# Kernel tuning notes

Hardware: AMD Instinct MI355X
Metric: run time of the kernel (lower is better)

Reference implementation:

```python
import jax, jax.numpy as jnp
import numpy as np

DEPTH = 16          # levels in the complete binary tree
D_IN = 256
H = 256
K = 2               # n_children
N_NODES = 2 ** DEPTH - 1  # 65535, heap/level order: children of node p at level l are (2p, 2p+1) at level l+1


def setup_inputs() -> dict:
    key = jax.random.key(0)
    ks = jax.random.split(key, 14)
    s = 0.05
    emb = jax.random.normal(ks[0], (N_NODES, D_IN), dtype=jnp.float32)
    mk = lambda k, shape: (jax.random.normal(k, shape, dtype=jnp.float32) * s)
    return {
        "emb": emb,
        "W_i": mk(ks[1], (H, D_IN)), "b_i": mk(ks[2], (H,)), "U_i": mk(ks[3], (K, H, H)),
        "W_o": mk(ks[4], (H, D_IN)), "b_o": mk(ks[5], (H,)), "U_o": mk(ks[6], (K, H, H)),
        "W_u": mk(ks[7], (H, D_IN)), "b_u": mk(ks[8], (H,)), "U_u": mk(ks[9], (K, H, H)),
        "W_f": mk(ks[10], (H, D_IN)), "b_f": mk(ks[11], (H,)), "U_f": mk(ks[12], (K, H, H)),
    }


def _node_batch(x, ch_h, ch_c, W_i, b_i, U_i, W_o, b_o, U_o, W_u, b_u, U_u, W_f, b_f, U_f):
    # x: [n, D_IN]; ch_h, ch_c: [n, K, H]
    # Linear: x @ W.T + b (torch layout W=[out,in]); U_k h = h @ U[k].T
    def gate(W, b, U):
        return x @ W.T + b + jnp.einsum("nkh,kdh->nd", ch_h, U)
    i = jax.nn.sigmoid(gate(W_i, b_i, U_i))
    o = jax.nn.sigmoid(gate(W_o, b_o, U_o))
    u = jnp.tanh(gate(W_u, b_u, U_u))
    # per-child forget gates: f_k = sigmoid(W_f x + U_f[k] h_k)
    f = jax.nn.sigmoid((x @ W_f.T + b_f)[:, None, :] + jnp.einsum("nkh,kdh->nkd", ch_h, U_f))
    c = i * u + jnp.sum(f * ch_c, axis=1)
    h = o * jnp.tanh(c)
    return h, c


def reference(emb, W_i, b_i, U_i, W_o, b_o, U_o, W_u, b_u, U_u, W_f, b_f, U_f):
    params = (W_i, b_i, U_i, W_o, b_o, U_o, W_u, b_u, U_u, W_f, b_f, U_f)
    # leaves: level DEPTH-1, zero children (matches zero-padding in node_forward)
    n = 2 ** (DEPTH - 1)
    start = n - 1
    zeros = jnp.zeros((n, K, H), dtype=emb.dtype)
    h, c = _node_batch(emb[start:start + n], zeros, zeros, *params)
    # bottom-up over internal levels; children of position p are (2p, 2p+1) in level below
    for l in range(DEPTH - 2, -1, -1):
        n = 2 ** l
        start = n - 1
        ch_h = h.reshape(n, K, H)
        ch_c = c.reshape(n, K, H)
        h, c = _node_batch(emb[start:start + n], ch_h, ch_c, *params)
    return h[0], c[0]  # root (hidden, cell), each [H]
```

## Files before the change

### kernel.cpp

```cpp
#include <hip/hip_runtime.h>
#include <hip/hip_bf16.h>
#include <cstdint>
#include <cstddef>


typedef __attribute__((ext_vector_type(8))) __bf16 bf16x8;
typedef __attribute__((ext_vector_type(4))) float floatx4;

#define TB 64

__device__ __forceinline__ float sigf(float x) { return 1.0f / (1.0f + __expf(-x)); }

__device__ __forceinline__ void load_lds16(const void* g, void* l) {
    __builtin_amdgcn_global_load_lds(
        (const __attribute__((address_space(1))) unsigned int*)g,
        (__attribute__((address_space(3))) unsigned int*)l, 16, 0, 0);
}

__global__ void pack_weights(const float* __restrict__ Wi, const float* __restrict__ bi, const float* __restrict__ Ui,
                             const float* __restrict__ Wo, const float* __restrict__ bo, const float* __restrict__ Uo,
                             const float* __restrict__ Wu, const float* __restrict__ bu, const float* __restrict__ Uu,
                             const float* __restrict__ Wf, const float* __restrict__ bf, const float* __restrict__ Uf,
                             __hip_bfloat16* __restrict__ Wpack, float* __restrict__ biasv)
{
    int m = blockIdx.x;
    int d = blockIdx.y;
    int k = threadIdx.x;
    const float* tbl[12] = {Wi, Wo, Wu, Wf,
                            Ui, Uo, Uu, Uf,
                            Ui + 65536, Uo + 65536, Uu + 65536, Uf + 65536};
    Wpack[((size_t)m * 256 + d) * 256 + k] = __float2bfloat16(tbl[m][d * 256 + k]);
    if (m < 4 && k == 0) {
        const float* bt[4] = {bi, bo, bu, bf};
        biasv[m * 256 + d] = bt[m][d];
    }
}

__global__ void convert_f32_bf16(const float* __restrict__ in, __hip_bfloat16* __restrict__ out, int n4)
{
    int i = blockIdx.x * 256 + threadIdx.x;
    if (i >= n4) return;
    float4 v = ((const float4*)in)[i];
    __hip_bfloat16 tmp[4];
    tmp[0] = __float2bfloat16(v.x);
    tmp[1] = __float2bfloat16(v.y);
    tmp[2] = __float2bfloat16(v.z);
    tmp[3] = __float2bfloat16(v.w);
    *(ushort4*)(out + (size_t)i * 4) = *(const ushort4*)tmp;
}

__global__ __launch_bounds__(256) void gemm_zx(
    const __hip_bfloat16* __restrict__ embB,
    const __hip_bfloat16* __restrict__ Wpack,
    const float* __restrict__ biasv,
    float* __restrict__ preZ,
    int M)
{
    __shared__ __hip_bfloat16 sA[64 * 32];
    __shared__ __hip_bfloat16 sB[64 * 32];
    const int t = threadIdx.x;
    const int s = blockIdx.x >> 2;
    const int d0 = (blockIdx.x & 3) * 64;
    const int bm0 = blockIdx.y * 64;
    const int lane = t & 63, w = t >> 6, lrow = lane & 15, q = lane >> 4;

    floatx4 acc[4];
    #pragma unroll
    for (int mt = 0; mt < 4; ++mt) acc[mt] = (floatx4){0.f, 0.f, 0.f, 0.f};

    for (int kk = 0; kk < 8; ++kk) {
        const int k0 = kk * 32;
        {
            int r = t >> 2, kc = t & 3;
            load_lds16(embB + (size_t)(bm0 + r) * 256 + k0 + kc * 8, &sA[t * 8]);
            load_lds16(Wpack + (size_t)(s * 256 + d0 + r) * 256 + k0 + kc * 8, &sB[t * 8]);
        }
        __syncthreads();
        bf16x8 af[4];
        #pragma unroll
        for (int mt = 0; mt < 4; ++mt)
            af[mt] = *(const bf16x8*)&sA[(mt * 16 + lrow) * 32 + q * 8];
        bf16x8 bfr = *(const bf16x8*)&sB[(w * 16 + lrow) * 32 + q * 8];
        #pragma unroll
        for (int mt = 0; mt < 4; ++mt)
            acc[mt] = __builtin_amdgcn_mfma_f32_16x16x32_bf16(af[mt], bfr, acc[mt], 0, 0, 0);
        __syncthreads();
    }

    const int d = d0 + w * 16 + lrow;
    const float bv = biasv[s * 256 + d];
    #pragma unroll
    for (int mt = 0; mt < 4; ++mt)
        #pragma unroll
        for (int rr = 0; rr < 4; ++rr) {
            int m = bm0 + mt * 16 + q * 4 + rr;
            if (m < M) preZ[(size_t)m * 1024 + s * 256 + d] = acc[mt][rr] + bv;
        }
}

template<int NS, int NP>
__global__ __launch_bounds__(256) void fused_level3(
    const __hip_bfloat16* __restrict__ embX,
    const __hip_bfloat16* __restrict__ hprev,
    const float* __restrict__ cprev,
    const __hip_bfloat16* __restrict__ Wpack,
    const float* __restrict__ biasv,
    __hip_bfloat16* __restrict__ hout,
    float* __restrict__ cout,
    int M)
{
    __shared__ __hip_bfloat16 sA[64 * 64];
    __shared__ __hip_bfloat16 sB[NS * 64 * 64];
    const int t = threadIdx.x;
    const int dchunk = blockIdx.x;
    const int bm0 = blockIdx.y * 64;
    const int lane = t & 63;
    const int w = t >> 6;
    const int lrow = lane & 15;
    const int q = lane >> 4;

    floatx4 accS[3][4];
    floatx4 accF[NP][4];
    #pragma unroll
    for (int s = 0; s < 3; ++s)
        #pragma unroll
        for (int mt = 0; mt < 4; ++mt) accS[s][mt] = (floatx4){0.f, 0.f, 0.f, 0.f};
    #pragma unroll
    for (int p = 0; p < NP; ++p)
        #pragma unroll
        for (int mt = 0; mt < 4; ++mt) accF[p][mt] = (floatx4){0.f, 0.f, 0.f, 0.f};

    #pragma unroll
    for (int p = 0; p < NP; ++p) {
        const __hip_bfloat16* Abase = (p == 0) ? embX : hprev;
        const int astride = (p == 0) ? 256 : 512;
        const int aoff = (p == 0) ? 0 : (p - 1) * 256;
        for (int kk = 0; kk < 4; ++kk) {
            const int k0 = kk * 64;
            #pragma unroll
            for (int rep = 0; rep < 2; ++rep) {
                int C = rep * 256 + t;
                int r = C >> 3, c0 = C & 7;
                load_lds16(Abase + (size_t)(bm0 + r) * astride + aoff + k0 + (c0 ^ (r & 7)) * 8,
                           &sA[C * 8]);
            }
            #pragma unroll
            for (int rep = 0; rep < NS * 2; ++rep) {
                int C = rep * 256 + t;
                int s = C >> 9, r = (C >> 3) & 63, c0 = C & 7;
                load_lds16(Wpack + (size_t)((p * 4 + s) * 256 + dchunk * 64 + r) * 256
                                 + k0 + (c0 ^ (r & 7)) * 8,
                           &sB[C * 8]);
            }
            __syncthreads();

            bf16x8 af[2][4];
            #pragma unroll
            for (int ks = 0; ks < 2; ++ks)
                #pragma unroll
                for (int mt = 0; mt < 4; ++mt)
                    af[ks][mt] = *(const bf16x8*)&sA[(mt * 16 + lrow) * 64
                                                     + (((ks * 4 + q) ^ (lrow & 7)) * 8)];
            #pragma unroll
            for (int s = 0; s < NS; ++s) {
                #pragma unroll
                for (int ks = 0; ks < 2; ++ks) {
                    bf16x8 bfr = *(const bf16x8*)&sB[(s * 64 + w * 16 + lrow) * 64
                                                     + (((ks * 4 + q) ^ (lrow & 7)) * 8)];
                    if (s < 3) {
                        #pragma unroll
                        for (int mt = 0; mt < 4; ++mt)
                            accS[s][mt] = __builtin_amdgcn_mfma_f32_16x16x32_bf16(af[ks][mt], bfr, accS[s][mt], 0, 0, 0);
                    } else {
                        #pragma unroll
                        for (int mt = 0; mt < 4; ++mt)
                            accF[p][mt] = __builtin_amdgcn_mfma_f32_16x16x32_bf16(af[ks][mt], bfr, accF[p][mt], 0, 0, 0);
                    }
                }
            }
            __syncthreads();
        }
    }

    const int d = dchunk * 64 + w * 16 + lrow;
    const float bI = biasv[d];
    const float bO = biasv[256 + d];
    const float bU = biasv[512 + d];
    const float bF = (NS == 4) ? biasv[768 + d] : 0.0f;
    #pragma unroll
    for (int mt = 0; mt < 4; ++mt) {
        #pragma unroll
        for (int rr = 0; rr < 4; ++rr) {
            const int m = bm0 + mt * 16 + q * 4 + rr;
            if (m >= M) continue;
            float iv = sigf(accS[0][mt][rr] + bI);
            float ov = sigf(accS[1][mt][rr] + bO);
            float uv = tanhf(accS[2][mt][rr] + bU);
            float c;
            if (NS == 4) {
                float fx = accF[0][mt][rr];
                float fl = sigf(fx + accF[NP >= 2 ? 1 : 0][mt][rr] + bF);
                float fr = sigf(fx + accF[NP >= 3 ? 2 : 0][mt][rr] + bF);
                c = iv * uv + fl * cprev[(size_t)m * 512 + d]
                            + fr * cprev[(size_t)m * 512 + 256 + d];
            } else {
                c = iv * uv;
            }
            cout[(size_t)m * 256 + d] = c;
            hout[(size_t)m * 256 + d] = __float2bfloat16(ov * tanhf(c));
        }
    }
}

__global__ __launch_bounds__(256) void tail_levels(
    __hip_bfloat16* __restrict__ hbuf, float* __restrict__ cbuf,
    const __hip_bfloat16* __restrict__ Wpack,
    const float* __restrict__ preZ,
    unsigned* __restrict__ bar, float* __restrict__ out)
{
    __shared__ __hip_bfloat16 sB[8 * 16 * 256];
    const int bid = blockIdx.x;
    const int t = threadIdx.x;
    const int dt = bid & 15;
    const int g = bid >> 4;
    const int w = t >> 6, lane = t & 63, lrow = lane & 15, q = lane >> 4;

    for (int rnd = 0; rnd < 16; ++rnd) {
        int C = rnd * 256 + t;
        int q8k = C & 31, r = (C >> 5) & 15, m8 = C >> 9;
        load_lds16(Wpack + (size_t)((4 + m8) * 256 + dt * 16 + r) * 256 + (q8k ^ (r & 7)) * 8,
                   &sB[(size_t)C * 8]);
    }
    __syncthreads();

    const int d = dt * 16 + lrow;
    unsigned barnum = 0;
    unsigned snum = 0;

    for (int l = 10; l >= 0; --l) {
        if (l <= 7 && g != 0) break;

        const int n = 1 << l;
        const int start = n - 1;
        const int startc = 2 * n - 1;
        const __hip_bfloat16* hp = hbuf + (size_t)startc * 256;
        const float* cp = cbuf + (size_t)startc * 256;
        __hip_bfloat16* ho = hbuf + (size_t)start * 256;
        float* co = cbuf + (size_t)start * 256;
        const int nmt = (n + 15) >> 4;
        const int slot   = (l > 7) ? (g * 4 + w) : w;
        const int stride = (l > 7) ? 16 : 4;

        for (int mt = slot; mt < nmt; mt += stride) {
            const int m0 = mt * 16;
            bf16x8 af[2][8];
            #pragma unroll
            for (int p = 0; p < 2; ++p)
                #pragma unroll
                for (int kk = 0; kk < 8; ++kk)
                    af[p][kk] = *(const bf16x8*)(hp + (size_t)(m0 + lrow) * 512 + p * 256 + kk * 32 + q * 8);
            float zi[4][4], clr[2][4];
            #pragma unroll
            for (int rr = 0; rr < 4; ++rr) {
                int m = m0 + q * 4 + rr;
                #pragma unroll
                for (int s = 0; s < 4; ++s)
                    zi[s][rr] = preZ[(size_t)(start + m) * 1024 + s * 256 + d];
                clr[0][rr] = cp[(size_t)m * 512 + d];
                clr[1][rr] = cp[(size_t)m * 512 + 256 + d];
            }

            floatx4 accS[3], accF1, accF2;
            #pragma unroll
            for (int s = 0; s < 3; ++s)
                accS[s] = (floatx4){zi[s][0], zi[s][1], zi[s][2], zi[s][3]};
            accF1 = (floatx4){0.f, 0.f, 0.f, 0.f};
            accF2 = (floatx4){0.f, 0.f, 0.f, 0.f};

            #pragma unroll
            for (int p = 0; p < 2; ++p)
                #pragma unroll
                for (int kk = 0; kk < 8; ++kk)
                    #pragma unroll
                    for (int s = 0; s < 4; ++s) {
                        bf16x8 bfr = *(const bf16x8*)&sB[((p * 4 + s) * 16 + lrow) * 256
                                                         + (((kk * 4 + q) ^ (lrow & 7)) * 8)];
                        if (s < 3)
                            accS[s] = __builtin_amdgcn_mfma_f32_16x16x32_bf16(af[p][kk], bfr, accS[s], 0, 0, 0);
                        else if (p == 0)
                            accF1 = __builtin_amdgcn_mfma_f32_16x16x32_bf16(af[p][kk], bfr, accF1, 0, 0, 0);
                        else
                            accF2 = __builtin_amdgcn_mfma_f32_16x16x32_bf16(af[p][kk], bfr, accF2, 0, 0, 0);
                    }

            #pragma unroll
            for (int rr = 0; rr < 4; ++rr) {
                int m = m0 + q * 4 + rr;
                if (m >= n) continue;
                float iv = sigf(accS[0][rr]);
                float ov = sigf(accS[1][rr]);
                float uv = tanhf(accS[2][rr]);
                float fx = zi[3][rr];
                float fl = sigf(fx + accF1[rr]);
                float fr = sigf(fx + accF2[rr]);
                float c = iv * uv + fl * clr[0][rr] + fr * clr[1][rr];
                float hv = ov * tanhf(c);
                if (l == 0) {
                    out[d] = hv;
                    out[256 + d] = c;
                } else {
                    co[(size_t)m * 256 + d] = c;
                    ho[(size_t)m * 256 + d] = __float2bfloat16(hv);
                }
            }
        }

        if (l > 0) {
            __syncthreads();
            if (l > 7) {
                ++barnum;
                if (t == 0) {
                    unsigned v = __hip_atomic_fetch_add(&bar[0], 1, __ATOMIC_ACQ_REL,
                                                        __HIP_MEMORY_SCOPE_AGENT) + 1;
                    if (v == barnum * 64u) {
                        __hip_atomic_fetch_add(&bar[64], 1, __ATOMIC_RELEASE,
                                               __HIP_MEMORY_SCOPE_AGENT);
                    } else {
                        while (__hip_atomic_load(&bar[64], __ATOMIC_RELAXED,
                                                 __HIP_MEMORY_SCOPE_AGENT) < barnum)
                            __builtin_amdgcn_s_sleep(1);
                    }
                }
            } else {
                ++snum;
                if (t == 0) {
                    unsigned v = __hip_atomic_fetch_add(&bar[128], 1, __ATOMIC_ACQ_REL,
                                                        __HIP_MEMORY_SCOPE_AGENT) + 1;
                    if (v == snum * 16u) {
                        __hip_atomic_fetch_add(&bar[192], 1, __ATOMIC_RELEASE,
                                               __HIP_MEMORY_SCOPE_AGENT);
                    } else {
                        while (__hip_atomic_load(&bar[192], __ATOMIC_RELAXED,
                                                 __HIP_MEMORY_SCOPE_AGENT) < snum)
                            __builtin_amdgcn_s_sleep(1);
                    }
                }
            }
            __syncthreads();
            __builtin_amdgcn_fence(__ATOMIC_ACQUIRE, "agent");
        }
    }
}

extern "C" void kernel_launch(void* const* d_in, const int* in_sizes, int n_in,
                              void* d_out, int out_size, void* d_ws, size_t ws_size,
                              hipStream_t stream)
{
    const float* emb = (const float*)d_in[0];
    const float* Wi  = (const float*)d_in[1];
    const float* bi  = (const float*)d_in[2];
    const float* Ui  = (const float*)d_in[3];
    const float* Wo  = (const float*)d_in[4];
    const float* bo  = (const float*)d_in[5];
    const float* Uo  = (const float*)d_in[6];
    const float* Wu  = (const float*)d_in[7];
    const float* bu  = (const float*)d_in[8];
    const float* Uu  = (const float*)d_in[9];
    const float* Wf  = (const float*)d_in[10];
    const float* bf  = (const float*)d_in[11];
    const float* Uf  = (const float*)d_in[12];

    char* p = (char*)d_ws;
    __hip_bfloat16* Wpack = (__hip_bfloat16*)p;  p += (size_t)12 * 256 * 256 * 2;
    float* biasv          = (float*)p;           p += (size_t)4 * 256 * 4;
    __hip_bfloat16* embB  = (__hip_bfloat16*)p;  p += (size_t)65535 * 256 * 2;
    __hip_bfloat16* hbuf  = (__hip_bfloat16*)p;  p += (size_t)65535 * 256 * 2;
    float* cbuf           = (float*)p;           p += (size_t)65535 * 256 * 4;
    float* preZ           = (float*)p;           p += (size_t)2047 * 1024 * 4;
    unsigned* bar         = (unsigned*)p;        p += 1024;

    hipMemsetAsync(bar, 0, 1024, stream);
    pack_weights<<<dim3(12, 256), 256, 0, stream>>>(Wi, bi, Ui, Wo, bo, Uo, Wu, bu, Uu, Wf, bf, Uf,
                                                    Wpack, biasv);
    convert_f32_bf16<<<(65535 * 256 / 4 + 255) / 256, 256, 0, stream>>>(emb, embB, 65535 * 256 / 4);

    gemm_zx<<<dim3(16, 32), 256, 0, stream>>>(embB, Wpack, biasv, preZ, 2047);

    {
        const int n = 32768, start = n - 1;
        fused_level3<3, 1><<<dim3(4, n / 64), 256, 0, stream>>>(
            embB + (size_t)start * 256, nullptr, nullptr, Wpack, biasv,
            hbuf + (size_t)start * 256, cbuf + (size_t)start * 256, n);
    }
    for (int l = 14; l >= 11; --l) {
        const int n = 1 << l;
        const int start = n - 1;
        const int startc = 2 * n - 1;
        fused_level3<4, 3><<<dim3(4, n / 64), 256, 0, stream>>>(
            embB + (size_t)start * 256,
            hbuf + (size_t)startc * 256,
            cbuf + (size_t)startc * 256,
            Wpack, biasv,
            hbuf + (size_t)start * 256, cbuf + (size_t)start * 256, n);
    }

    tail_levels<<<TB, 256, 0, stream>>>(hbuf, cbuf, Wpack, preZ, bar, (float*)d_out);
}
```

Before: 394.9 us.

## Merge setup kernels, co-launch leaf level with x-GEMM, extend persistent tail

Folds weight packing, embedding conversion and barrier reset into one setup launch, replacing a memset and two kernels. The leaf-level fused kernel and the input-projection GEMM now share one launch, and that GEMM covers levels 12 and below instead of 10 and below. The persistent tail kernel starts at level 12, so two fewer per-level launches are needed. The cost is a larger precomputed buffer, and levels 12 and 11 now run inside only 64 persistent blocks instead of full-grid launches.

```diff
diff --git a/kernel.cpp b/kernel.cpp
--- a/kernel.cpp
+++ b/kernel.cpp
@@ -17,89 +17,48 @@
         (__attribute__((address_space(3))) unsigned int*)l, 16, 0, 0);
 }
 
-__global__ void pack_weights(const float* __restrict__ Wi, const float* __restrict__ bi, const float* __restrict__ Ui,
-                             const float* __restrict__ Wo, const float* __restrict__ bo, const float* __restrict__ Uo,
-                             const float* __restrict__ Wu, const float* __restrict__ bu, const float* __restrict__ Uu,
-                             const float* __restrict__ Wf, const float* __restrict__ bf, const float* __restrict__ Uf,
-                             __hip_bfloat16* __restrict__ Wpack, float* __restrict__ biasv)
-{
-    int m = blockIdx.x;
-    int d = blockIdx.y;
-    int k = threadIdx.x;
-    const float* tbl[12] = {Wi, Wo, Wu, Wf,
-                            Ui, Uo, Uu, Uf,
-                            Ui + 65536, Uo + 65536, Uu + 65536, Uf + 65536};
-    Wpack[((size_t)m * 256 + d) * 256 + k] = __float2bfloat16(tbl[m][d * 256 + k]);
-    if (m < 4 && k == 0) {
-        const float* bt[4] = {bi, bo, bu, bf};
-        biasv[m * 256 + d] = bt[m][d];
-    }
-}
-
-__global__ void convert_f32_bf16(const float* __restrict__ in, __hip_bfloat16* __restrict__ out, int n4)
-{
-    int i = blockIdx.x * 256 + threadIdx.x;
-    if (i >= n4) return;
-    float4 v = ((const float4*)in)[i];
-    __hip_bfloat16 tmp[4];
-    tmp[0] = __float2bfloat16(v.x);
-    tmp[1] = __float2bfloat16(v.y);
-    tmp[2] = __float2bfloat16(v.z);
-    tmp[3] = __float2bfloat16(v.w);
-    *(ushort4*)(out + (size_t)i * 4) = *(const ushort4*)tmp;
-}
-
-__global__ __launch_bounds__(256) void gemm_zx(
-    const __hip_bfloat16* __restrict__ embB,
-    const __hip_bfloat16* __restrict__ Wpack,
-    const float* __restrict__ biasv,
-    float* __restrict__ preZ,
-    int M)
-{
-    __shared__ __hip_bfloat16 sA[64 * 32];
-    __shared__ __hip_bfloat16 sB[64 * 32];
+#define NB_PACK 3072
+#define NB_CONV 16385
+__global__ void setup(const float* __restrict__ Wi, const float* __restrict__ bi, const float* __restrict__ Ui,
+                      const float* __restrict__ Wo, const float* __restrict__ bo, const float* __restrict__ Uo,
+                      const float* __restrict__ Wu, const float* __restrict__ bu, const float* __restrict__ Uu,
+                      const float* __restrict__ Wf, const float* __restrict__ bf, const float* __restrict__ Uf,
+                      __hip_bfloat16* __restrict__ Wpack, float* __restrict__ biasv,
+                      const float* __restrict__ emb, __hip_bfloat16* __restrict__ embB,
+                      unsigned* __restrict__ bar)
+{
+    const int bid = blockIdx.x;
     const int t = threadIdx.x;
-    const int s = blockIdx.x >> 2;
-    const int d0 = (blockIdx.x & 3) * 64;
-    const int bm0 = blockIdx.y * 64;
-    const int lane = t & 63, w = t >> 6, lrow = lane & 15, q = lane >> 4;
-
-    floatx4 acc[4];
-    #pragma unroll
-    for (int mt = 0; mt < 4; ++mt) acc[mt] = (floatx4){0.f, 0.f, 0.f, 0.f};
-
-    for (int kk = 0; kk < 8; ++kk) {
-        const int k0 = kk * 32;
-        {
-            int r = t >> 2, kc = t & 3;
-            load_lds16(embB + (size_t)(bm0 + r) * 256 + k0 + kc * 8, &sA[t * 8]);
-            load_lds16(Wpack + (size_t)(s * 256 + d0 + r) * 256 + k0 + kc * 8, &sB[t * 8]);
-        }
-        __syncthreads();
-        bf16x8 af[4];
-        #pragma unroll
-        for (int mt = 0; mt < 4; ++mt)
-            af[mt] = *(const bf16x8*)&sA[(mt * 16 + lrow) * 32 + q * 8];
-        bf16x8 bfr = *(const bf16x8*)&sB[(w * 16 + lrow) * 32 + q * 8];
-        #pragma unroll
-        for (int mt = 0; mt < 4; ++mt)
-            acc[mt] = __builtin_amdgcn_mfma_f32_16x16x32_bf16(af[mt], bfr, acc[mt], 0, 0, 0);
-        __syncthreads();
-    }
-
-    const int d = d0 + w * 16 + lrow;
-    const float bv = biasv[s * 256 + d];
-    #pragma unroll
-    for (int mt = 0; mt < 4; ++mt)
-        #pragma unroll
-        for (int rr = 0; rr < 4; ++rr) {
-            int m = bm0 + mt * 16 + q * 4 + rr;
-            if (m < M) preZ[(size_t)m * 1024 + s * 256 + d] = acc[mt][rr] + bv;
-        }
+    if (bid < NB_PACK) {
+        int m = bid >> 8, d = bid & 255, k = t;
+        const float* tbl[12] = {Wi, Wo, Wu, Wf,
+                                Ui, Uo, Uu, Uf,
+                                Ui + 65536, Uo + 65536, Uu + 65536, Uf + 65536};
+        Wpack[((size_t)m * 256 + d) * 256 + k] = __float2bfloat16(tbl[m][d * 256 + k]);
+        if (m < 4 && k == 0) {
+            const float* bt[4] = {bi, bo, bu, bf};
+            biasv[m * 256 + d] = bt[m][d];
+        }
+    } else if (bid < NB_PACK + NB_CONV) {
+        int i = (bid - NB_PACK) * 256 + t;
+        if (i < 65535 * 256 / 4) {
+            float4 v = ((const float4*)emb)[i];
+            __hip_bfloat16 tmp[4];
+            tmp[0] = __float2bfloat16(v.x);
+            tmp[1] = __float2bfloat16(v.y);
+            tmp[2] = __float2bfloat16(v.z);
+            tmp[3] = __float2bfloat16(v.w);
+            *(ushort4*)(embB + (size_t)i * 4) = *(const ushort4*)tmp;
+        }
+    } else {
+        bar[t] = 0;
+    }
 }
 
 template<int NS, int NP>
-__global__ __launch_bounds__(256) void fused_level3(
+__device__ __forceinline__ void fused_body(
+    __hip_bfloat16* sA, __hip_bfloat16* sB,
+    int dchunk, int bm0,
     const __hip_bfloat16* __restrict__ embX,
     const __hip_bfloat16* __restrict__ hprev,
     const float* __restrict__ cprev,
@@ -109,11 +68,7 @@
     float* __restrict__ cout,
     int M)
 {
-    __shared__ __hip_bfloat16 sA[64 * 64];
-    __shared__ __hip_bfloat16 sB[NS * 64 * 64];
     const int t = threadIdx.x;
-    const int dchunk = blockIdx.x;
-    const int bm0 = blockIdx.y * 64;
     const int lane = t & 63;
     const int w = t >> 6;
     const int lrow = lane & 15;
@@ -212,6 +167,95 @@
     }
 }
 
+__device__ __forceinline__ void gemm_body(
+    __hip_bfloat16* sA, __hip_bfloat16* sB,
+    int s, int d0, int bm0,
+    const __hip_bfloat16* __restrict__ embB,
+    const __hip_bfloat16* __restrict__ Wpack,
+    const float* __restrict__ biasv,
+    float* __restrict__ preZ,
+    int M)
+{
+    const int t = threadIdx.x;
+    const int lane = t & 63, w = t >> 6, lrow = lane & 15, q = lane >> 4;
+
+    floatx4 acc[4];
+    #pragma unroll
+    for (int mt = 0; mt < 4; ++mt) acc[mt] = (floatx4){0.f, 0.f, 0.f, 0.f};
+
+    for (int kk = 0; kk < 8; ++kk) {
+        const int k0 = kk * 32;
+        {
+            int r = t >> 2, kc = t & 3;
+            load_lds16(embB + (size_t)(bm0 + r) * 256 + k0 + kc * 8, &sA[t * 8]);
+            load_lds16(Wpack + (size_t)(s * 256 + d0 + r) * 256 + k0 + kc * 8, &sB[t * 8]);
+        }
+        __syncthreads();
+        bf16x8 af[4];
+        #pragma unroll
+        for (int mt = 0; mt < 4; ++mt)
+            af[mt] = *(const bf16x8*)&sA[(mt * 16 + lrow) * 32 + q * 8];
+        bf16x8 bfr = *(const bf16x8*)&sB[(w * 16 + lrow) * 32 + q * 8];
+        #pragma unroll
+        for (int mt = 0; mt < 4; ++mt)
+            acc[mt] = __builtin_amdgcn_mfma_f32_16x16x32_bf16(af[mt], bfr, acc[mt], 0, 0, 0);
+        __syncthreads();
+    }
+
+    const int d = d0 + w * 16 + lrow;
+    const float bv = biasv[s * 256 + d];
+    #pragma unroll
+    for (int mt = 0; mt < 4; ++mt)
+        #pragma unroll
+        for (int rr = 0; rr < 4; ++rr) {
+            int m = bm0 + mt * 16 + q * 4 + rr;
+            if (m < M) preZ[(size_t)m * 1024 + s * 256 + d] = acc[mt][rr] + bv;
+        }
+}
+
+__global__ __launch_bounds__(256) void leaves_gemm(
+    const __hip_bfloat16* __restrict__ embB,
+    const __hip_bfloat16* __restrict__ Wpack,
+    const float* __restrict__ biasv,
+    float* __restrict__ preZ,
+    __hip_bfloat16* __restrict__ hbuf,
+    float* __restrict__ cbuf)
+{
+    __shared__ __hip_bfloat16 smem[16384];
+    const int bid = blockIdx.x;
+    if (bid < 2048) {
+        const int n = 32768, start = n - 1;
+        fused_body<3, 1>(smem, smem + 4096,
+                         bid & 3, (bid >> 2) * 64,
+                         embB + (size_t)start * 256, nullptr, nullptr,
+                         Wpack, biasv,
+                         hbuf + (size_t)start * 256, cbuf + (size_t)start * 256, n);
+    } else {
+        const int gid = bid - 2048;
+        const int x = gid & 15;
+        gemm_body(smem, smem + 2048,
+                  x >> 2, (x & 3) * 64, (gid >> 4) * 64,
+                  embB, Wpack, biasv, preZ, 8191);
+    }
+}
+
+template<int NS, int NP>
+__global__ __launch_bounds__(256) void fused_level3(
+    const __hip_bfloat16* __restrict__ embX,
+    const __hip_bfloat16* __restrict__ hprev,
+    const float* __restrict__ cprev,
+    const __hip_bfloat16* __restrict__ Wpack,
+    const float* __restrict__ biasv,
+    __hip_bfloat16* __restrict__ hout,
+    float* __restrict__ cout,
+    int M)
+{
+    __shared__ __hip_bfloat16 sA[64 * 64];
+    __shared__ __hip_bfloat16 sB[NS * 64 * 64];
+    fused_body<NS, NP>(sA, sB, blockIdx.x, blockIdx.y * 64,
+                       embX, hprev, cprev, Wpack, biasv, hout, cout, M);
+}
+
 __global__ __launch_bounds__(256) void tail_levels(
     __hip_bfloat16* __restrict__ hbuf, float* __restrict__ cbuf,
     const __hip_bfloat16* __restrict__ Wpack,
@@ -237,7 +281,7 @@
     unsigned barnum = 0;
     unsigned snum = 0;
 
-    for (int l = 10; l >= 0; --l) {
+    for (int l = 12; l >= 0; --l) {
         if (l <= 7 && g != 0) break;
 
         const int n = 1 << l;
@@ -376,23 +420,16 @@
     __hip_bfloat16* embB  = (__hip_bfloat16*)p;  p += (size_t)65535 * 256 * 2;
     __hip_bfloat16* hbuf  = (__hip_bfloat16*)p;  p += (size_t)65535 * 256 * 2;
     float* cbuf           = (float*)p;           p += (size_t)65535 * 256 * 4;
-    float* preZ           = (float*)p;           p += (size_t)2047 * 1024 * 4;
+    float* preZ           = (float*)p;           p += (size_t)8191 * 1024 * 4;
     unsigned* bar         = (unsigned*)p;        p += 1024;
 
-    hipMemsetAsync(bar, 0, 1024, stream);
-    pack_weights<<<dim3(12, 256), 256, 0, stream>>>(Wi, bi, Ui, Wo, bo, Uo, Wu, bu, Uu, Wf, bf, Uf,
-                                                    Wpack, biasv);
-    convert_f32_bf16<<<(65535 * 256 / 4 + 255) / 256, 256, 0, stream>>>(emb, embB, 65535 * 256 / 4);
-
-    gemm_zx<<<dim3(16, 32), 256, 0, stream>>>(embB, Wpack, biasv, preZ, 2047);
-
-    {
-        const int n = 32768, start = n - 1;
-        fused_level3<3, 1><<<dim3(4, n / 64), 256, 0, stream>>>(
-            embB + (size_t)start * 256, nullptr, nullptr, Wpack, biasv,
-            hbuf + (size_t)start * 256, cbuf + (size_t)start * 256, n);
-    }
-    for (int l = 14; l >= 11; --l) {
+    setup<<<NB_PACK + NB_CONV + 1, 256, 0, stream>>>(
+        Wi, bi, Ui, Wo, bo, Uo, Wu, bu, Uu, Wf, bf, Uf,
+        Wpack, biasv, emb, embB, bar);
+
+    leaves_gemm<<<4096, 256, 0, stream>>>(embB, Wpack, biasv, preZ, hbuf, cbuf);
+
+    for (int l = 14; l >= 13; --l) {
         const int n = 1 << l;
         const int start = n - 1;
         const int startc = 2 * n - 1;
```

After: 471.6 us. +19.4%, slower.
